# Kernel optimization log

Measured on AMD Instinct MI355X. Metric: run time of the kernel, lower is better.

Reference implementation:

```python
import jax, jax.numpy as jnp
import numpy as np

B, N, H = 32, 2048, 512
MASK_NEG = 1e30  # matches torch mask_logic constant


def setup_inputs() -> dict:
    key = jax.random.key(0)
    ks = jax.random.split(key, 10)
    Q = jax.random.normal(ks[0], (B, H), dtype=jnp.float32)
    K = jax.random.normal(ks[1], (B, N, H), dtype=jnp.float32)
    V = jax.random.normal(ks[2], (B, N, H), dtype=jnp.float32)
    adj = jax.random.randint(ks[3], (B, N), 0, 2, dtype=jnp.int32)
    s_mask = jax.random.randint(ks[4], (B, N), 0, 2, dtype=jnp.int32)
    s = 1.0 / np.sqrt(H)
    w_att = jax.random.uniform(ks[5], (1, 2 * H), jnp.float32, -s, s)  # nn.Linear(2H,1) weight
    b_att = jax.random.uniform(ks[6], (1,), jnp.float32, -s, s)
    Wr0 = jax.random.uniform(ks[7], (H, H), jnp.float32, -s, s)
    Wr1 = jax.random.uniform(ks[8], (H, H), jnp.float32, -s, s)
    Wri = jax.random.uniform(ks[9], (H, H), jnp.float32, -s, s)
    return {"Q": Q, "K": K, "V": V, "adj": adj, "s_mask": s_mask,
            "w_att": w_att, "b_att": b_att, "Wr0": Wr0, "Wr1": Wr1, "Wri": Wri}


def reference(Q, K, V, adj, s_mask, w_att, b_att, Wr0, Wr1, Wri):
    Hdim = Q.shape[-1]
    # additive score: linear(cat(Q_exp, K)) split into Q-part + K-part (avoids materializing [B,N,2H])
    wq, wk = w_att[:, :Hdim], w_att[:, Hdim:]          # [1,H] each
    alpha = (Q @ wq[0]) [:, None] + K @ wk[0] + b_att[0]  # [B,N]
    # adjacency mask + softmax over neighbors
    masked = alpha - (1.0 - adj.astype(jnp.float32)) * MASK_NEG
    attn = jax.nn.softmax(masked, axis=1)               # [B,N]
    # gated value projection: V0 where s_mask==1, V1 where 0
    V0 = jnp.einsum('bnh,oh->bno', V, Wr0)
    V1 = jnp.einsum('bnh,oh->bno', V, Wr1)
    sm = s_mask.astype(jnp.float32)[..., None]          # [B,N,1]
    Vm = V0 * sm + V1 * (1.0 - sm)
    # weighted aggregation + residual projection
    attn_sum = jnp.einsum('bn,bnh->bh', attn, Vm) + Q @ Wri.T
    return attn[:, None, :], attn_sum                   # ([B,1,N], [B,H])
```

## Files before the change

### kernel.cpp

```cpp
#include <hip/hip_runtime.h>

#define BB 32
#define NN 2048
#define HH 512

static __device__ __forceinline__ float dot4(float4 a, float4 b) {
    return a.x * b.x + a.y * b.y + a.z * b.z + a.w * b.w;
}


__global__ void k_scores(const float* __restrict__ K,
                         const float* __restrict__ w_att,
                         const int* __restrict__ adj,
                         float* __restrict__ scores,
                         float* __restrict__ ws) {
    int gtid = blockIdx.x * blockDim.x + threadIdx.x;
    if (gtid < 2 * BB * HH) ws[gtid] = 0.0f;
    int wave = gtid >> 6;
    int lane = threadIdx.x & 63;
    if (wave >= BB * NN) return;
    const float* wk = w_att + HH;
    size_t base = (size_t)wave * HH;
    float4 k0 = *(const float4*)(K + base + lane * 4);
    float4 k1 = *(const float4*)(K + base + 256 + lane * 4);
    float4 a0 = *(const float4*)(wk + lane * 4);
    float4 a1 = *(const float4*)(wk + 256 + lane * 4);
    float s = dot4(k0, a0) + dot4(k1, a1);
#pragma unroll
    for (int off = 32; off > 0; off >>= 1) s += __shfl_down(s, off, 64);
    if (lane == 0) scores[wave] = adj[wave] ? s : -1e30f;
}

__global__ void k_wsum(const float* __restrict__ V,
                       const float* __restrict__ scores,
                       float* __restrict__ attn,
                       const int* __restrict__ s_mask,
                       float* __restrict__ u0,
                       float* __restrict__ u1) {
    int b = blockIdx.x >> 4;
    int n0 = (blockIdx.x & 15) * 128;
    int t = threadIdx.x;
    int h4 = (t & 127) * 4;
    int half = t >> 7;
    __shared__ float red[4];
    __shared__ float w0s[128], w1s[128], comb[1024];

    const float* srow = scores + b * NN;
    float v[8];
    float m = -INFINITY;
#pragma unroll
    for (int i = 0; i < 8; i++) {
        v[i] = srow[t * 8 + i];
        m = fmaxf(m, v[i]);
    }
#pragma unroll
    for (int off = 32; off > 0; off >>= 1) m = fmaxf(m, __shfl_xor(m, off, 64));
    if ((t & 63) == 0) red[t >> 6] = m;
    __syncthreads();
    float m4 = fmaxf(fmaxf(red[0], red[1]), fmaxf(red[2], red[3]));
    float sum = 0.0f;
#pragma unroll
    for (int i = 0; i < 8; i++) sum += expf(v[i] - m4);
#pragma unroll
    for (int off = 32; off > 0; off >>= 1) sum += __shfl_xor(sum, off, 64);
    __syncthreads();
    if ((t & 63) == 0) red[t >> 6] = sum;
    __syncthreads();
    float inv = 1.0f / (red[0] + red[1] + red[2] + red[3]);

    if (t < 128) {
        float w = expf(srow[n0 + t] - m4) * inv;
        attn[b * NN + n0 + t] = w;
        int sm = s_mask[b * NN + n0 + t];
        w0s[t] = sm ? w : 0.0f;
        w1s[t] = sm ? 0.0f : w;
    }
    __syncthreads();

    float4 a0 = {0, 0, 0, 0}, a1 = {0, 0, 0, 0};
    const float* Vb = V + ((size_t)(b * NN + n0 + half * 64)) * HH + h4;
#pragma unroll 4
    for (int i = 0; i < 64; i++) {
        float4 x = *(const float4*)(Vb + (size_t)i * HH);
        float w0 = w0s[half * 64 + i];
        float w1 = w1s[half * 64 + i];
        a0.x += w0 * x.x; a0.y += w0 * x.y; a0.z += w0 * x.z; a0.w += w0 * x.w;
        a1.x += w1 * x.x; a1.y += w1 * x.y; a1.z += w1 * x.z; a1.w += w1 * x.w;
    }
    if (half == 1) {
        int i8 = (t - 128) * 8;
        comb[i8 + 0] = a0.x; comb[i8 + 1] = a0.y; comb[i8 + 2] = a0.z; comb[i8 + 3] = a0.w;
        comb[i8 + 4] = a1.x; comb[i8 + 5] = a1.y; comb[i8 + 6] = a1.z; comb[i8 + 7] = a1.w;
    }
    __syncthreads();
    if (half == 0) {
        int i8 = t * 8;
        a0.x += comb[i8 + 0]; a0.y += comb[i8 + 1]; a0.z += comb[i8 + 2]; a0.w += comb[i8 + 3];
        a1.x += comb[i8 + 4]; a1.y += comb[i8 + 5]; a1.z += comb[i8 + 6]; a1.w += comb[i8 + 7];
        float* p0 = u0 + b * HH + h4;
        float* p1 = u1 + b * HH + h4;
        atomicAdd(p0 + 0, a0.x); atomicAdd(p0 + 1, a0.y);
        atomicAdd(p0 + 2, a0.z); atomicAdd(p0 + 3, a0.w);
        atomicAdd(p1 + 0, a1.x); atomicAdd(p1 + 1, a1.y);
        atomicAdd(p1 + 2, a1.z); atomicAdd(p1 + 3, a1.w);
    }
}

__global__ void k_out(const float* __restrict__ Q,
                      const float* __restrict__ Wr0,
                      const float* __restrict__ Wr1,
                      const float* __restrict__ Wri,
                      const float* __restrict__ u0,
                      const float* __restrict__ u1,
                      float* __restrict__ out) {
    int wave = (blockIdx.x * blockDim.x + threadIdx.x) >> 6;
    int lane = threadIdx.x & 63;
    if (wave >= BB * HH) return;
    int b = wave >> 9;
    int o = wave & 511;
    const float* q = Q + b * HH;
    const float* x0 = u0 + b * HH;
    const float* x1 = u1 + b * HH;
    const float* r0 = Wr0 + (size_t)o * HH;
    const float* r1 = Wr1 + (size_t)o * HH;
    const float* ri = Wri + (size_t)o * HH;
    float s = 0.0f;
#pragma unroll
    for (int part = 0; part < 2; part++) {
        int h = part * 256 + lane * 4;
        s += dot4(*(const float4*)(r0 + h), *(const float4*)(x0 + h));
        s += dot4(*(const float4*)(r1 + h), *(const float4*)(x1 + h));
        s += dot4(*(const float4*)(ri + h), *(const float4*)(q + h));
    }
#pragma unroll
    for (int off = 32; off > 0; off >>= 1) s += __shfl_down(s, off, 64);
    if (lane == 0) out[wave] = s;
}

extern "C" void kernel_launch(void* const* d_in, const int* in_sizes, int n_in,
                              void* d_out, int out_size, void* d_ws, size_t ws_size,
                              hipStream_t stream) {
    const float* Q = (const float*)d_in[0];
    const float* K = (const float*)d_in[1];
    const float* V = (const float*)d_in[2];
    const int* adj = (const int*)d_in[3];
    const int* s_mask = (const int*)d_in[4];
    const float* w_att = (const float*)d_in[5];
    const float* Wr0 = (const float*)d_in[7];
    const float* Wr1 = (const float*)d_in[8];
    const float* Wri = (const float*)d_in[9];

    float* out = (float*)d_out;
    float* attn = out;
    float* attn_sum = out + BB * NN;
    float* ws = (float*)d_ws;
    float* u0 = ws;
    float* u1 = ws + BB * HH;
    float* scores = ws + 2 * BB * HH;

    k_scores<<<(BB * NN) / 4, 256, 0, stream>>>(K, w_att, adj, scores, ws);
    k_wsum<<<BB * 16, 256, 0, stream>>>(V, scores, attn, s_mask, u0, u1);
    k_out<<<(BB * HH) / 4, 256, 0, stream>>>(Q, Wr0, Wr1, Wri, u0, u1, attn_sum);
}
```

Before: 301.7 us.

## Split weighted sum over hidden-dim chunks, drop atomics, batch score rows per wave

```diff
diff --git a/kernel.cpp b/kernel.cpp
--- a/kernel.cpp
+++ b/kernel.cpp
@@ -12,55 +12,73 @@
 __global__ void k_scores(const float* __restrict__ K,
                          const float* __restrict__ w_att,
                          const int* __restrict__ adj,
-                         float* __restrict__ scores,
-                         float* __restrict__ ws) {
-    int gtid = blockIdx.x * blockDim.x + threadIdx.x;
-    if (gtid < 2 * BB * HH) ws[gtid] = 0.0f;
-    int wave = gtid >> 6;
+                         float* __restrict__ scores) {
+    int wave = (blockIdx.x * blockDim.x + threadIdx.x) >> 6;
     int lane = threadIdx.x & 63;
-    if (wave >= BB * NN) return;
     const float* wk = w_att + HH;
-    size_t base = (size_t)wave * HH;
-    float4 k0 = *(const float4*)(K + base + lane * 4);
-    float4 k1 = *(const float4*)(K + base + 256 + lane * 4);
     float4 a0 = *(const float4*)(wk + lane * 4);
     float4 a1 = *(const float4*)(wk + 256 + lane * 4);
-    float s = dot4(k0, a0) + dot4(k1, a1);
-#pragma unroll
-    for (int off = 32; off > 0; off >>= 1) s += __shfl_down(s, off, 64);
-    if (lane == 0) scores[wave] = adj[wave] ? s : -1e30f;
-}
-
+    int row0 = wave * 4;
+    const float* Kb = K + (size_t)row0 * HH + lane * 4;
+    float4 k00 = *(const float4*)(Kb);
+    float4 k01 = *(const float4*)(Kb + 256);
+    float4 k10 = *(const float4*)(Kb + HH);
+    float4 k11 = *(const float4*)(Kb + HH + 256);
+    float4 k20 = *(const float4*)(Kb + 2 * HH);
+    float4 k21 = *(const float4*)(Kb + 2 * HH + 256);
+    float4 k30 = *(const float4*)(Kb + 3 * HH);
+    float4 k31 = *(const float4*)(Kb + 3 * HH + 256);
+    float s0 = dot4(k00, a0) + dot4(k01, a1);
+    float s1 = dot4(k10, a0) + dot4(k11, a1);
+    float s2 = dot4(k20, a0) + dot4(k21, a1);
+    float s3 = dot4(k30, a0) + dot4(k31, a1);
+#pragma unroll
+    for (int off = 32; off > 0; off >>= 1) {
+        s0 += __shfl_down(s0, off, 64);
+        s1 += __shfl_down(s1, off, 64);
+        s2 += __shfl_down(s2, off, 64);
+        s3 += __shfl_down(s3, off, 64);
+    }
+    if (lane == 0) {
+        int4 a = *(const int4*)(adj + row0);
+        float4 o;
+        o.x = a.x ? s0 : -1e30f;
+        o.y = a.y ? s1 : -1e30f;
+        o.z = a.z ? s2 : -1e30f;
+        o.w = a.w ? s3 : -1e30f;
+        *(float4*)(scores + row0) = o;
+    }
+}
+
+#define CH 16
 __global__ void k_wsum(const float* __restrict__ V,
                        const float* __restrict__ scores,
                        float* __restrict__ attn,
                        const int* __restrict__ s_mask,
                        float* __restrict__ u0,
                        float* __restrict__ u1) {
-    int b = blockIdx.x >> 4;
-    int n0 = (blockIdx.x & 15) * 128;
+    int b = blockIdx.x >> 5;
+    int hc = (blockIdx.x & 31) * CH;
     int t = threadIdx.x;
-    int h4 = (t & 127) * 4;
-    int half = t >> 7;
     __shared__ float red[4];
-    __shared__ float w0s[128], w1s[128], comb[1024];
+    __shared__ float2 wls[NN];
+    __shared__ float part[4][4][8];
 
     const float* srow = scores + b * NN;
-    float v[8];
-    float m = -INFINITY;
-#pragma unroll
-    for (int i = 0; i < 8; i++) {
-        v[i] = srow[t * 8 + i];
-        m = fmaxf(m, v[i]);
-    }
+    float4 va = *(const float4*)(srow + t * 8);
+    float4 vb = *(const float4*)(srow + t * 8 + 4);
+    float m = fmaxf(fmaxf(fmaxf(va.x, va.y), fmaxf(va.z, va.w)),
+                    fmaxf(fmaxf(vb.x, vb.y), fmaxf(vb.z, vb.w)));
 #pragma unroll
     for (int off = 32; off > 0; off >>= 1) m = fmaxf(m, __shfl_xor(m, off, 64));
     if ((t & 63) == 0) red[t >> 6] = m;
     __syncthreads();
     float m4 = fmaxf(fmaxf(red[0], red[1]), fmaxf(red[2], red[3]));
-    float sum = 0.0f;
-#pragma unroll
-    for (int i = 0; i < 8; i++) sum += expf(v[i] - m4);
+    float e0 = expf(va.x - m4), e1 = expf(va.y - m4);
+    float e2 = expf(va.z - m4), e3 = expf(va.w - m4);
+    float e4 = expf(vb.x - m4), e5 = expf(vb.y - m4);
+    float e6 = expf(vb.z - m4), e7 = expf(vb.w - m4);
+    float sum = ((e0 + e1) + (e2 + e3)) + ((e4 + e5) + (e6 + e7));
 #pragma unroll
     for (int off = 32; off > 0; off >>= 1) sum += __shfl_xor(sum, off, 64);
     __syncthreads();
@@ -68,41 +86,63 @@
     __syncthreads();
     float inv = 1.0f / (red[0] + red[1] + red[2] + red[3]);
 
-    if (t < 128) {
-        float w = expf(srow[n0 + t] - m4) * inv;
-        attn[b * NN + n0 + t] = w;
-        int sm = s_mask[b * NN + n0 + t];
-        w0s[t] = sm ? w : 0.0f;
-        w1s[t] = sm ? 0.0f : w;
-    }
-    __syncthreads();
-
-    float4 a0 = {0, 0, 0, 0}, a1 = {0, 0, 0, 0};
-    const float* Vb = V + ((size_t)(b * NN + n0 + half * 64)) * HH + h4;
-#pragma unroll 4
-    for (int i = 0; i < 64; i++) {
-        float4 x = *(const float4*)(Vb + (size_t)i * HH);
-        float w0 = w0s[half * 64 + i];
-        float w1 = w1s[half * 64 + i];
-        a0.x += w0 * x.x; a0.y += w0 * x.y; a0.z += w0 * x.z; a0.w += w0 * x.w;
-        a1.x += w1 * x.x; a1.y += w1 * x.y; a1.z += w1 * x.z; a1.w += w1 * x.w;
-    }
-    if (half == 1) {
-        int i8 = (t - 128) * 8;
-        comb[i8 + 0] = a0.x; comb[i8 + 1] = a0.y; comb[i8 + 2] = a0.z; comb[i8 + 3] = a0.w;
-        comb[i8 + 4] = a1.x; comb[i8 + 5] = a1.y; comb[i8 + 6] = a1.z; comb[i8 + 7] = a1.w;
-    }
-    __syncthreads();
-    if (half == 0) {
-        int i8 = t * 8;
-        a0.x += comb[i8 + 0]; a0.y += comb[i8 + 1]; a0.z += comb[i8 + 2]; a0.w += comb[i8 + 3];
-        a1.x += comb[i8 + 4]; a1.y += comb[i8 + 5]; a1.z += comb[i8 + 6]; a1.w += comb[i8 + 7];
-        float* p0 = u0 + b * HH + h4;
-        float* p1 = u1 + b * HH + h4;
-        atomicAdd(p0 + 0, a0.x); atomicAdd(p0 + 1, a0.y);
-        atomicAdd(p0 + 2, a0.z); atomicAdd(p0 + 3, a0.w);
-        atomicAdd(p1 + 0, a1.x); atomicAdd(p1 + 1, a1.y);
-        atomicAdd(p1 + 2, a1.z); atomicAdd(p1 + 3, a1.w);
+    float w0 = e0 * inv, w1 = e1 * inv, w2 = e2 * inv, w3 = e3 * inv;
+    float w4 = e4 * inv, w5 = e5 * inv, w6 = e6 * inv, w7 = e7 * inv;
+    if (hc == 0) {
+        float4 oa = {w0, w1, w2, w3};
+        float4 ob = {w4, w5, w6, w7};
+        *(float4*)(attn + b * NN + t * 8) = oa;
+        *(float4*)(attn + b * NN + t * 8 + 4) = ob;
+    }
+    int4 sa = *(const int4*)(s_mask + b * NN + t * 8);
+    int4 sb = *(const int4*)(s_mask + b * NN + t * 8 + 4);
+    int i8 = t * 8;
+    wls[i8 + 0] = sa.x ? make_float2(w0, 0.f) : make_float2(0.f, w0);
+    wls[i8 + 1] = sa.y ? make_float2(w1, 0.f) : make_float2(0.f, w1);
+    wls[i8 + 2] = sa.z ? make_float2(w2, 0.f) : make_float2(0.f, w2);
+    wls[i8 + 3] = sa.w ? make_float2(w3, 0.f) : make_float2(0.f, w3);
+    wls[i8 + 4] = sb.x ? make_float2(w4, 0.f) : make_float2(0.f, w4);
+    wls[i8 + 5] = sb.y ? make_float2(w5, 0.f) : make_float2(0.f, w5);
+    wls[i8 + 6] = sb.z ? make_float2(w6, 0.f) : make_float2(0.f, w6);
+    wls[i8 + 7] = sb.w ? make_float2(w7, 0.f) : make_float2(0.f, w7);
+    __syncthreads();
+
+    int col = t & 3;
+    int rowg = t >> 2;
+    const float* Vb = V + (size_t)b * NN * HH + hc + col * 4;
+    float4 A0 = {0, 0, 0, 0}, A1 = {0, 0, 0, 0};
+#pragma unroll 8
+    for (int i = 0; i < 32; i++) {
+        int n = rowg + (i << 6);
+        float4 x = *(const float4*)(Vb + (size_t)n * HH);
+        float2 w = wls[n];
+        A0.x += w.x * x.x; A0.y += w.x * x.y; A0.z += w.x * x.z; A0.w += w.x * x.w;
+        A1.x += w.y * x.x; A1.y += w.y * x.y; A1.z += w.y * x.z; A1.w += w.y * x.w;
+    }
+#pragma unroll
+    for (int off = 32; off >= 4; off >>= 1) {
+        A0.x += __shfl_down(A0.x, off, 64); A0.y += __shfl_down(A0.y, off, 64);
+        A0.z += __shfl_down(A0.z, off, 64); A0.w += __shfl_down(A0.w, off, 64);
+        A1.x += __shfl_down(A1.x, off, 64); A1.y += __shfl_down(A1.y, off, 64);
+        A1.z += __shfl_down(A1.z, off, 64); A1.w += __shfl_down(A1.w, off, 64);
+    }
+    int wv = t >> 6;
+    if ((t & 63) < 4) {
+        float* p = part[wv][t & 3];
+        p[0] = A0.x; p[1] = A0.y; p[2] = A0.z; p[3] = A0.w;
+        p[4] = A1.x; p[5] = A1.y; p[6] = A1.z; p[7] = A1.w;
+    }
+    __syncthreads();
+    if (t < 4) {
+        float4 r0 = {0, 0, 0, 0}, r1 = {0, 0, 0, 0};
+#pragma unroll
+        for (int w = 0; w < 4; w++) {
+            const float* p = part[w][t];
+            r0.x += p[0]; r0.y += p[1]; r0.z += p[2]; r0.w += p[3];
+            r1.x += p[4]; r1.y += p[5]; r1.z += p[6]; r1.w += p[7];
+        }
+        *(float4*)(u0 + b * HH + hc + t * 4) = r0;
+        *(float4*)(u1 + b * HH + hc + t * 4) = r1;
     }
 }
 
@@ -158,7 +198,7 @@
     float* u1 = ws + BB * HH;
     float* scores = ws + 2 * BB * HH;
 
-    k_scores<<<(BB * NN) / 4, 256, 0, stream>>>(K, w_att, adj, scores, ws);
-    k_wsum<<<BB * 16, 256, 0, stream>>>(V, scores, attn, s_mask, u0, u1);
+    k_scores<<<(BB * NN) / 16, 256, 0, stream>>>(K, w_att, adj, scores);
+    k_wsum<<<BB * (HH / CH), 256, 0, stream>>>(V, scores, attn, s_mask, u0, u1);
     k_out<<<(BB * HH) / 4, 256, 0, stream>>>(Q, Wr0, Wr1, Wri, u0, u1, attn_sum);
 }
```

Result: slower. 313.7 us (+4.0%).
